# Kernel tuning notes

Measured on AMD Instinct MI355X. Metric: run time of the kernel, lower is better.

The kernel has to match this reference:

```python
import jax, jax.numpy as jnp
import numpy as np

B, S, D, H = 4, 1024, 1024, 16
DH = D // H  # 64
SCALE = 1.0 / np.sqrt(D)  # module uses 1/sqrt(d_model), not d_head


def _mh(t):
    # [B,S,D] -> [B*H,S,DH]
    b, s, _ = t.shape
    return t.reshape(b, s, H, DH).transpose(0, 2, 1, 3).reshape(b * H, s, DH)


def _shift(t):
    # pad one zero at FRONT of last dim, reinterpret (row-major) as [BH,L+1,S], drop first row
    bh, s, l = t.shape
    t = jnp.concatenate([jnp.zeros((bh, s, 1), t.dtype), t], axis=-1)
    return t.reshape(bh, l + 1, s)[:, 1:, :]


def setup_inputs() -> dict:
    key = jax.random.key(0)
    ks = jax.random.split(key, 12)
    w_sc = 1.0 / np.sqrt(D)
    return {
        "x": jax.random.normal(ks[0], (B, S, D), jnp.float32),
        "u": jax.random.normal(ks[1], (DH,), jnp.float32) * 0.02,
        "v": jax.random.normal(ks[2], (DH,), jnp.float32) * 0.02,
        "pos": jax.random.normal(ks[3], (B, S, D), jnp.float32),
        "Wq": jax.random.normal(ks[4], (D, D), jnp.float32) * w_sc,
        "bq": jnp.zeros((D,), jnp.float32),
        "Wk": jax.random.normal(ks[5], (D, D), jnp.float32) * w_sc,
        "bk": jnp.zeros((D,), jnp.float32),
        "Wv": jax.random.normal(ks[6], (D, D), jnp.float32) * w_sc,
        "bv": jnp.zeros((D,), jnp.float32),
        "Wc": jax.random.normal(ks[7], (D, D), jnp.float32) * w_sc,
        "bc": jnp.zeros((D,), jnp.float32),
    }


def reference(x, u, v, pos, Wq, bq, Wk, bk, Wv, bv, Wc, bc):
    q = _mh(x @ Wq.T + bq)      # [BH,S,DH]
    k = _mh(x @ Wk.T + bk)      # [BH,S,DH]
    w = _mh(x @ Wv.T + bv)      # [BH,S,DH]
    r = _mh(pos)                # [BH,S,DH]
    ac = jnp.einsum('bjk,bmk->bjm', q + u, k)          # content-content  [BH,S,S]
    bd = _shift(jnp.einsum('bjk,blk->bjl', q + v, r))  # content-position [BH,S,S]
    att = jax.nn.softmax((ac + bd) * SCALE, axis=-1)   # dropout is identity (eval)
    o = att @ w                                        # [BH,S,DH]
    o = o.reshape(B, H, S, DH).transpose(0, 2, 1, 3).reshape(B, S, D)
    return o @ Wc.T + bc
```

## Files before the change

kernel.cpp:

```cpp
#include <hip/hip_runtime.h>
#include <hip/hip_bf16.h>


typedef __bf16 bf16x8 __attribute__((ext_vector_type(8)));
typedef float  f32x4  __attribute__((ext_vector_type(4)));
typedef unsigned short u16x4 __attribute__((ext_vector_type(4)));

struct alignas(16) U128 { unsigned long long lo, hi; };

__device__ __forceinline__ bf16x8 ldg8(const __hip_bfloat16* p) {
    U128 u = *reinterpret_cast<const U128*>(p);
    return __builtin_bit_cast(bf16x8, u);
}

__device__ __forceinline__ __bf16 f2b(float f) {
    __hip_bfloat16 h = __float2bfloat16(f);
    return __builtin_bit_cast(__bf16, h);
}
__device__ __forceinline__ unsigned short f2bu(float f) {
    __hip_bfloat16 h = __float2bfloat16(f);
    return __builtin_bit_cast(unsigned short, h);
}
__device__ __forceinline__ float b2f(__bf16 b) {
    __hip_bfloat16 h = __builtin_bit_cast(__hip_bfloat16, b);
    return __bfloat162float(h);
}
__device__ __forceinline__ float bu2f(unsigned short u) {
    __hip_bfloat16 h = __builtin_bit_cast(__hip_bfloat16, u);
    return __bfloat162float(h);
}

__device__ __forceinline__ bf16x8 ldg8cvt(const float* p) {
    f32x4 a = *reinterpret_cast<const f32x4*>(p);
    f32x4 b = *reinterpret_cast<const f32x4*>(p + 4);
    bf16x8 r;
    r[0] = f2b(a[0]); r[1] = f2b(a[1]); r[2] = f2b(a[2]); r[3] = f2b(a[3]);
    r[4] = f2b(b[0]); r[5] = f2b(b[1]); r[6] = f2b(b[2]); r[7] = f2b(b[3]);
    return r;
}

#define MFMA16(a, b, c) __builtin_amdgcn_mfma_f32_16x16x32_bf16((a), (b), (c), 0, 0, 0)

#define C1F 0.0450843334f

__device__ __forceinline__ void gll16(const __hip_bfloat16* g, void* lds_wave_base) {
    __builtin_amdgcn_global_load_lds(
        (const __attribute__((address_space(1))) void*)g,
        (__attribute__((address_space(3))) void*)lds_wave_base,
        16, 0, 0);
}

__global__ __launch_bounds__(256) void cvt_kernel(
    const float* __restrict__ x,  const float* __restrict__ pos,
    const float* __restrict__ wq, const float* __restrict__ wk,
    const float* __restrict__ wv, const float* __restrict__ wc,
    __hip_bfloat16* __restrict__ xb, __hip_bfloat16* __restrict__ posb,
    __hip_bfloat16* __restrict__ wqkvb, __hip_bfloat16* __restrict__ wcb)
{
    const size_t base = ((size_t)blockIdx.x * 256 + threadIdx.x) * 8;
    const size_t M1 = (size_t)1 << 20;
    const float* src; __hip_bfloat16* dst; size_t o;
    if (base < 4*M1)        { src = x;   dst = xb;           o = base; }
    else if (base < 8*M1)   { src = pos; dst = posb;         o = base - 4*M1; }
    else if (base < 9*M1)   { src = wq;  dst = wqkvb;        o = base - 8*M1; }
    else if (base < 10*M1)  { src = wk;  dst = wqkvb + M1;   o = base - 9*M1; }
    else if (base < 11*M1)  { src = wv;  dst = wqkvb + 2*M1; o = base - 10*M1; }
    else                    { src = wc;  dst = wcb;          o = base - 11*M1; }
    *(bf16x8*)(dst + o) = ldg8cvt(src + o);
}

__global__ __launch_bounds__(256) void gemm_qkv(
    const __hip_bfloat16* __restrict__ A,
    const __hip_bfloat16* __restrict__ Bm,
    const float* __restrict__ bq, const float* __restrict__ bk,
    const float* __restrict__ bv, const float* __restrict__ u,
    __hip_bfloat16* __restrict__ Qu,
    __hip_bfloat16* __restrict__ Kb, __hip_bfloat16* __restrict__ Vt)
{
    __shared__ __hip_bfloat16 As[128 * 32];
    __shared__ __hip_bfloat16 Bs[128 * 32];

    const int tid  = threadIdx.x;
    const int lane = tid & 63, w = tid >> 6;
    const int quad = lane >> 4, c16 = lane & 15;
    const int wm = w >> 1, wn = w & 1;
    const int m0 = blockIdx.y * 128;
    const int n0 = blockIdx.x * 128;

    const int srow = w * 16 + (lane >> 2);
    const int scol = (lane & 3) * 8;
    const __hip_bfloat16* gA0 = A  + (size_t)(m0 + srow) * 1024 + scol;
    const __hip_bfloat16* gA1 = gA0 + (size_t)64 * 1024;
    const __hip_bfloat16* gB0 = Bm + (size_t)(n0 + srow) * 1024 + scol;
    const __hip_bfloat16* gB1 = gB0 + (size_t)64 * 1024;
    char* ldsA0 = (char*)As + (w << 10);
    char* ldsA1 = ldsA0 + 4096;
    char* ldsB0 = (char*)Bs + (w << 10);
    char* ldsB1 = ldsB0 + 4096;

    f32x4 acc[4][4] = {};

    for (int k0 = 0; k0 < 1024; k0 += 32) {
        gll16(gA0 + k0, ldsA0);
        gll16(gA1 + k0, ldsA1);
        gll16(gB0 + k0, ldsB0);
        gll16(gB1 + k0, ldsB1);
        __syncthreads();

        bf16x8 af[4], bfr[4];
        #pragma unroll
        for (int i = 0; i < 4; ++i) {
            af[i]  = *(const bf16x8*)&As[(wm * 64 + i * 16 + c16) * 32 + quad * 8];
            bfr[i] = *(const bf16x8*)&Bs[(wn * 64 + i * 16 + c16) * 32 + quad * 8];
        }
        #pragma unroll
        for (int mi = 0; mi < 4; ++mi)
            #pragma unroll
            for (int ni = 0; ni < 4; ++ni)
                acc[mi][ni] = MFMA16(af[mi], bfr[ni], acc[mi][ni]);
        __syncthreads();
    }

    #pragma unroll
    for (int mi = 0; mi < 4; ++mi) {
        #pragma unroll
        for (int ni = 0; ni < 4; ++ni) {
            const int m = m0 + wm * 64 + mi * 16 + quad * 4;
            const int n = n0 + wn * 64 + ni * 16 + c16;
            if (n < 1024) {
                const float b0 = bq[n] + u[n & 63];
                #pragma unroll
                for (int r = 0; r < 4; ++r)
                    Qu[(size_t)(m + r) * 1024 + n] =
                        __float2bfloat16((acc[mi][ni][r] + b0) * C1F);
            } else if (n < 2048) {
                const int nn = n - 1024;
                const float b0 = bk[nn];
                #pragma unroll
                for (int r = 0; r < 4; ++r)
                    Kb[(size_t)(m + r) * 1024 + nn] =
                        __float2bfloat16(acc[mi][ni][r] + b0);
            } else {
                const int nn = n - 2048;
                const float b0 = bv[nn];
                const int d = nn & 63, hh = nn >> 6;
                const int bb = m >> 10, s = m & 1023;
                u16x4 pk;
                #pragma unroll
                for (int r = 0; r < 4; ++r)
                    pk[r] = f2bu(acc[mi][ni][r] + b0);
                *(u16x4*)&Vt[(((size_t)(bb * 16 + hh) * 64 + d) << 10) + s] = pk;
            }
        }
    }
}

__global__ __launch_bounds__(256) void gemm_fin64(
    const __hip_bfloat16* __restrict__ A,
    const __hip_bfloat16* __restrict__ Bm,
    float* __restrict__ dout, const float* __restrict__ bc)
{
    __shared__ __hip_bfloat16 As[64 * 32];
    __shared__ __hip_bfloat16 Bs[64 * 32];

    const int tid  = threadIdx.x;
    const int lane = tid & 63, w = tid >> 6;
    const int quad = lane >> 4, c16 = lane & 15;
    const int wm = w >> 1, wn = w & 1;
    const int m0 = blockIdx.y * 64;
    const int n0 = blockIdx.x * 64;

    const int srow = w * 16 + (lane >> 2);
    const int scol = (lane & 3) * 8;
    const __hip_bfloat16* gA = A  + (size_t)(m0 + srow) * 1024 + scol;
    const __hip_bfloat16* gB = Bm + (size_t)(n0 + srow) * 1024 + scol;
    char* ldsA = (char*)As + (w << 10);
    char* ldsB = (char*)Bs + (w << 10);

    f32x4 acc[2][2] = {};

    for (int k0 = 0; k0 < 1024; k0 += 32) {
        gll16(gA + k0, ldsA);
        gll16(gB + k0, ldsB);
        __syncthreads();

        bf16x8 af[2], bfr[2];
        #pragma unroll
        for (int i = 0; i < 2; ++i) {
            af[i]  = *(const bf16x8*)&As[(wm * 32 + i * 16 + c16) * 32 + quad * 8];
            bfr[i] = *(const bf16x8*)&Bs[(wn * 32 + i * 16 + c16) * 32 + quad * 8];
        }
        #pragma unroll
        for (int mi = 0; mi < 2; ++mi)
            #pragma unroll
            for (int ni = 0; ni < 2; ++ni)
                acc[mi][ni] = MFMA16(af[mi], bfr[ni], acc[mi][ni]);
        __syncthreads();
    }

    #pragma unroll
    for (int mi = 0; mi < 2; ++mi) {
        #pragma unroll
        for (int ni = 0; ni < 2; ++ni) {
            const int m = m0 + wm * 32 + mi * 16 + quad * 4;
            const int n = n0 + wn * 32 + ni * 16 + c16;
            const float b0 = bc[n];
            #pragma unroll
            for (int r = 0; r < 4; ++r)
                dout[(size_t)(m + r) * 1024 + n] = acc[mi][ni][r] + b0;
        }
    }
}

__device__ __forceinline__ int lidx16(int row, int c) {
    return (row << 10) + ((((c >> 3) ^ row) << 3) | (c & 7));
}

__global__ __launch_bounds__(512, 2) void attn_kernel(
    const __hip_bfloat16* __restrict__ Qu,
    const __hip_bfloat16* __restrict__ Kb,
    const __hip_bfloat16* __restrict__ Posb,
    const __hip_bfloat16* __restrict__ Vt,
    const float* __restrict__ uvec, const float* __restrict__ vvec,
    __hip_bfloat16* __restrict__ O)
{
    __shared__ __attribute__((aligned(16))) __hip_bfloat16 Ls[64 * 1024];
    __shared__ float Wsum[64 * 8];
    __shared__ float rs[64];

    const int tid  = threadIdx.x;
    const int lane = tid & 63, w = tid >> 6;
    const int quad = lane >> 4, c16 = lane & 15;
    const int i0 = blockIdx.y * 64;
    const int bh = blockIdx.x;
    const int b = bh >> 4, h = bh & 15;
    const size_t headoff = (size_t)h * 64;
    const size_t tokbase = (size_t)b * 1024;
    const int j2 = i0 + 64;
    const bool havej2 = (j2 < 1024);

    if (tid < 64) {
        const int i = i0 + tid;
        if (i + 1 < 1024) Ls[lidx16(tid, i + 1)] = __float2bfloat16(0.f);
    }

    const __hip_bfloat16* qup0 =
        Qu + (tokbase + i0 + c16) * 1024 + headoff + quad * 8;

    float dvuA[8], dvuB[8];
    #pragma unroll
    for (int j = 0; j < 8; ++j) {
        const int d = quad * 8 + j;
        dvuA[j] = (vvec[d]      - uvec[d])      * C1F;
        dvuB[j] = (vvec[d + 32] - uvec[d + 32]) * C1F;
    }
    bf16x8 au[4][2], av[4][2];
    #pragma unroll
    for (int g = 0; g < 4; ++g) {
        au[g][0] = ldg8(qup0 + (size_t)g * 16 * 1024);
        au[g][1] = ldg8(qup0 + (size_t)g * 16 * 1024 + 32);
        #pragma unroll
        for (int j = 0; j < 8; ++j) {
            av[g][0][j] = f2b(b2f(au[g][0][j]) + dvuA[j]);
            av[g][1][j] = f2b(b2f(au[g][1][j]) + dvuB[j]);
        }
    }

    {
        bf16x8 a4[2];
        if (havej2) {
            a4[0] = ldg8(qup0 + (size_t)64 * 1024);
            a4[1] = ldg8(qup0 + (size_t)64 * 1024 + 32);
            #pragma unroll
            for (int j = 0; j < 8; ++j) {
                a4[0][j] = f2b(b2f(a4[0][j]) + dvuA[j]);
                a4[1][j] = f2b(b2f(a4[1][j]) + dvuB[j]);
            }
        }
        for (int t = 0; t < 8; ++t) {
            const int l0 = w * 128 + t * 16;
            const __hip_bfloat16* rp =
                Posb + (tokbase + l0 + c16) * 1024 + headoff + quad * 8;
            const bf16x8 r0 = ldg8(rp);
            const bf16x8 r1 = ldg8(rp + 32);
            const int lq = l0 + quad * 4;
            #pragma unroll
            for (int g = 0; g < 4; ++g) {
                f32x4 c = (f32x4){0.f, 0.f, 0.f, 0.f};
                c = MFMA16(r0, av[g][0], c);
                c = MFMA16(r1, av[g][1], c);
                const int jl = g * 16 + c16;
                const int base2 = lq + i0 + jl + 1;
                const int rwm1 = jl - 1;
                #pragma unroll
                for (int r = 0; r < 4; ++r) {
                    const int t1 = base2 + r;
                    const int cc = t1 & 1023;
                    const int rw = rwm1 + (t1 >> 10);
                    if (rw >= 0)
                        Ls[lidx16(rw, cc)] = __float2bfloat16(c[r]);
                }
            }
            if (havej2) {
                f32x4 c = (f32x4){0.f, 0.f, 0.f, 0.f};
                c = MFMA16(r0, a4[0], c);
                c = MFMA16(r1, a4[1], c);
                if (c16 == 0) {
                    #pragma unroll
                    for (int r = 0; r < 4; ++r) {
                        const int cc = lq + r + i0 + 65;
                        if (cc < 1024)
                            Ls[lidx16(63, cc)] = __float2bfloat16(c[r]);
                    }
                }
            }
        }
    }
    __syncthreads();

    {
        float rsum[4] = {0.f, 0.f, 0.f, 0.f};
        for (int t = 0; t < 8; ++t) {
            const int c0 = w * 128 + t * 16;
            const __hip_bfloat16* kp =
                Kb + (tokbase + c0 + c16) * 1024 + headoff + quad * 8;
            const bf16x8 k0 = ldg8(kp);
            const bf16x8 k1 = ldg8(kp + 32);
            const int cc0 = c0 + quad * 4;
            #pragma unroll
            for (int g = 0; g < 4; ++g) {
                f32x4 c = (f32x4){0.f, 0.f, 0.f, 0.f};
                c = MFMA16(k0, au[g][0], c);
                c = MFMA16(k1, au[g][1], c);
                const int jl = g * 16 + c16;
                const int idx = lidx16(jl, cc0);
                const u16x4 bd = *(const u16x4*)&Ls[idx];
                u16x4 pk;
                float s4 = 0.f;
                #pragma unroll
                for (int r = 0; r < 4; ++r) {
                    const float p =
                        __builtin_amdgcn_exp2f(bu2f(bd[r]) + c[r]);
                    s4 += p;
                    pk[r] = f2bu(p);
                }
                *(u16x4*)&Ls[idx] = pk;
                rsum[g] += s4;
            }
        }
        #pragma unroll
        for (int g = 0; g < 4; ++g) {
            float s = rsum[g];
            s += __shfl_xor(s, 16);
            s += __shfl_xor(s, 32);
            if (lane < 16) Wsum[(g * 16 + lane) * 8 + w] = s;
        }
    }
    __syncthreads();

    if (tid < 64) {
        float s = 0.f;
        #pragma unroll
        for (int k = 0; k < 8; ++k) s += Wsum[tid * 8 + k];
        rs[tid] = 1.f / s;
    }
    __syncthreads();

    {
        const int d0 = (w & 3) * 16;
        const int kh = w >> 2;
        const __hip_bfloat16* vp =
            Vt + ((size_t)bh * 64 + d0 + c16) * 1024 + quad * 8;
        f32x4 acc[4] = {};
        for (int kk = kh * 512; kk < kh * 512 + 512; kk += 32) {
            const bf16x8 vld = ldg8(vp + kk);
            #pragma unroll
            for (int g = 0; g < 4; ++g) {
                const bf16x8 p =
                    *(const bf16x8*)&Ls[lidx16(g * 16 + c16, kk + quad * 8)];
                acc[g] = MFMA16(p, vld, acc[g]);
            }
        }
        __syncthreads();
        float* Lf = (float*)Ls;
        const int sbase = (w & 3) * 1024;
        if (kh == 1) {
            #pragma unroll
            for (int g = 0; g < 4; ++g)
                #pragma unroll
                for (int r = 0; r < 4; ++r)
                    Lf[sbase + g * 256 + (quad * 4 + r) * 16 + c16] = acc[g][r];
        }
        __syncthreads();
        if (kh == 0) {
            #pragma unroll
            for (int g = 0; g < 4; ++g)
                #pragma unroll
                for (int r = 0; r < 4; ++r) {
                    const int il = g * 16 + quad * 4 + r;
                    const float val =
                        (acc[g][r] + Lf[sbase + g * 256 + (quad * 4 + r) * 16 + c16])
                        * rs[il];
                    const int i = i0 + il;
                    const int d = d0 + c16;
                    O[(tokbase + i) * 1024 + headoff + d] = __float2bfloat16(val);
                }
        }
    }
}

extern "C" void kernel_launch(void* const* d_in, const int* in_sizes, int n_in,
                              void* d_out, int out_size, void* d_ws, size_t ws_size,
                              hipStream_t stream)
{
    const float* x   = (const float*)d_in[0];
    const float* u   = (const float*)d_in[1];
    const float* v   = (const float*)d_in[2];
    const float* pos = (const float*)d_in[3];
    const float* Wq  = (const float*)d_in[4];
    const float* bq  = (const float*)d_in[5];
    const float* Wk  = (const float*)d_in[6];
    const float* bk  = (const float*)d_in[7];
    const float* Wv  = (const float*)d_in[8];
    const float* bv  = (const float*)d_in[9];
    const float* Wc  = (const float*)d_in[10];
    const float* bc  = (const float*)d_in[11];

    const size_t MB = (size_t)1 << 20;
    char* ws = (char*)d_ws;
    __hip_bfloat16* Qu    = (__hip_bfloat16*)(ws + 0 * MB);
    __hip_bfloat16* Kb    = (__hip_bfloat16*)(ws + 8 * MB);
    __hip_bfloat16* Vt    = (__hip_bfloat16*)(ws + 16 * MB);
    __hip_bfloat16* xb    = (__hip_bfloat16*)(ws + 24 * MB);
    __hip_bfloat16* O     = (__hip_bfloat16*)(ws + 24 * MB);
    __hip_bfloat16* Posb  = (__hip_bfloat16*)(ws + 32 * MB);
    __hip_bfloat16* Wqkvb = (__hip_bfloat16*)(ws + 40 * MB);
    __hip_bfloat16* Wcb   = (__hip_bfloat16*)(ws + 46 * MB);

    cvt_kernel<<<6144, 256, 0, stream>>>(x, pos, Wq, Wk, Wv, Wc,
                                         xb, Posb, Wqkvb, Wcb);

    gemm_qkv<<<dim3(24, 32), dim3(256), 0, stream>>>(
        xb, Wqkvb, bq, bk, bv, u, Qu, Kb, Vt);

    attn_kernel<<<dim3(64, 16), dim3(512), 0, stream>>>(
        Qu, Kb, Posb, Vt, u, v, O);

    gemm_fin64<<<dim3(16, 64), dim3(256), 0, stream>>>(
        O, Wcb, (float*)d_out, bc);
}
```

Before: 255.7 us.

## Split attention score buffer into two column halves to halve LDS footprint

The attention kernel now builds the 64x1024 shifted-position/probability tile in two 512-column phases, so the shared buffer shrinks from 128KB to 64KB. Launch bounds rise from two to four blocks per CU so more blocks can be resident. Each phase recomputes the needed position-score tiles (about 36 of 64 per phase, split unevenly across waves) and accumulates P·V across phases, with the row-sum normalisation deferred to the end. In exchange it repeats the Q/u/v loads, does some redundant position MFMAs, adds more barriers, and the higher launch bound may cause register pressure or spills.

```diff
diff --git a/kernel.cpp b/kernel.cpp
--- a/kernel.cpp
+++ b/kernel.cpp
@@ -212,11 +212,11 @@
     }
 }
 
-__device__ __forceinline__ int lidx16(int row, int c) {
-    return (row << 10) + ((((c >> 3) ^ row) << 3) | (c & 7));
-}
-
-__global__ __launch_bounds__(512, 2) void attn_kernel(
+__device__ __forceinline__ int lidx9(int row, int c) {
+    return (row << 9) + ((((c >> 3) ^ row) << 3) | (c & 7));
+}
+
+__global__ __launch_bounds__(512, 4) void attn_kernel(
     const __hip_bfloat16* __restrict__ Qu,
     const __hip_bfloat16* __restrict__ Kb,
     const __hip_bfloat16* __restrict__ Posb,
@@ -224,7 +224,7 @@
     const float* __restrict__ uvec, const float* __restrict__ vvec,
     __hip_bfloat16* __restrict__ O)
 {
-    __shared__ __attribute__((aligned(16))) __hip_bfloat16 Ls[64 * 1024];
+    __shared__ __attribute__((aligned(16))) __hip_bfloat16 Ls[64 * 512];
     __shared__ float Wsum[64 * 8];
     __shared__ float rs[64];
 
@@ -239,34 +239,46 @@
     const int j2 = i0 + 64;
     const bool havej2 = (j2 < 1024);
 
-    if (tid < 64) {
-        const int i = i0 + tid;
-        if (i + 1 < 1024) Ls[lidx16(tid, i + 1)] = __float2bfloat16(0.f);
-    }
-
     const __hip_bfloat16* qup0 =
         Qu + (tokbase + i0 + c16) * 1024 + headoff + quad * 8;
 
-    float dvuA[8], dvuB[8];
-    #pragma unroll
-    for (int j = 0; j < 8; ++j) {
-        const int d = quad * 8 + j;
-        dvuA[j] = (vvec[d]      - uvec[d])      * C1F;
-        dvuB[j] = (vvec[d + 32] - uvec[d + 32]) * C1F;
-    }
-    bf16x8 au[4][2], av[4][2];
-    #pragma unroll
-    for (int g = 0; g < 4; ++g) {
-        au[g][0] = ldg8(qup0 + (size_t)g * 16 * 1024);
-        au[g][1] = ldg8(qup0 + (size_t)g * 16 * 1024 + 32);
+    const int ntile = (w < 5) ? 5 : 4;
+    const int tbase = (w < 5) ? w * 5 : 25 + (w - 5) * 4;
+
+    f32x4 obacc[4] = {};
+    float rsum[4] = {0.f, 0.f, 0.f, 0.f};
+    const int d0 = (w & 3) * 16;
+    const int kh = w >> 2;
+    const __hip_bfloat16* vp =
+        Vt + ((size_t)bh * 64 + d0 + c16) * 1024 + quad * 8;
+
+    for (int ph = 0; ph < 2; ++ph) {
+        const int h0 = ph << 9;
+
+        if (tid < 64) {
+            const int c = i0 + tid + 1;
+            if (c < 1024 && ((c ^ h0) & 512) == 0)
+                Ls[lidx9(tid, c & 511)] = __float2bfloat16(0.f);
+        }
+
+        float dvuA[8], dvuB[8];
         #pragma unroll
         for (int j = 0; j < 8; ++j) {
-            av[g][0][j] = f2b(b2f(au[g][0][j]) + dvuA[j]);
-            av[g][1][j] = f2b(b2f(au[g][1][j]) + dvuB[j]);
-        }
-    }
-
-    {
+            const int d = quad * 8 + j;
+            dvuA[j] = (vvec[d]      - uvec[d])      * C1F;
+            dvuB[j] = (vvec[d + 32] - uvec[d + 32]) * C1F;
+        }
+        bf16x8 au[4][2], av[4][2];
+        #pragma unroll
+        for (int g = 0; g < 4; ++g) {
+            au[g][0] = ldg8(qup0 + (size_t)g * 16 * 1024);
+            au[g][1] = ldg8(qup0 + (size_t)g * 16 * 1024 + 32);
+            #pragma unroll
+            for (int j = 0; j < 8; ++j) {
+                av[g][0][j] = f2b(b2f(au[g][0][j]) + dvuA[j]);
+                av[g][1][j] = f2b(b2f(au[g][1][j]) + dvuB[j]);
+            }
+        }
         bf16x8 a4[2];
         if (havej2) {
             a4[0] = ldg8(qup0 + (size_t)64 * 1024);
@@ -277,8 +289,11 @@
                 a4[1][j] = f2b(b2f(a4[1][j]) + dvuB[j]);
             }
         }
-        for (int t = 0; t < 8; ++t) {
-            const int l0 = w * 128 + t * 16;
+
+        const int Tstart = ((h0 - i0 - 65) & 1023) >> 4;
+        for (int s = 0; s < ntile; ++s) {
+            const int tl = (Tstart + tbase + s) & 63;
+            const int l0 = tl << 4;
             const __hip_bfloat16* rp =
                 Posb + (tokbase + l0 + c16) * 1024 + headoff + quad * 8;
             const bf16x8 r0 = ldg8(rp);
@@ -297,8 +312,8 @@
                     const int t1 = base2 + r;
                     const int cc = t1 & 1023;
                     const int rw = rwm1 + (t1 >> 10);
-                    if (rw >= 0)
-                        Ls[lidx16(rw, cc)] = __float2bfloat16(c[r]);
+                    if (rw >= 0 && ((cc ^ h0) & 512) == 0)
+                        Ls[lidx9(rw, cc & 511)] = __float2bfloat16(c[r]);
                 }
             }
             if (havej2) {
@@ -308,32 +323,29 @@
                 if (c16 == 0) {
                     #pragma unroll
                     for (int r = 0; r < 4; ++r) {
-                        const int cc = lq + r + i0 + 65;
-                        if (cc < 1024)
-                            Ls[lidx16(63, cc)] = __float2bfloat16(c[r]);
+                        const int t1 = lq + r + j2 + 1;
+                        if (t1 < 1024 && ((t1 ^ h0) & 512) == 0)
+                            Ls[lidx9(63, t1 & 511)] = __float2bfloat16(c[r]);
                     }
                 }
             }
         }
-    }
-    __syncthreads();
-
-    {
-        float rsum[4] = {0.f, 0.f, 0.f, 0.f};
-        for (int t = 0; t < 8; ++t) {
-            const int c0 = w * 128 + t * 16;
+        __syncthreads();
+
+        for (int t = 0; t < 4; ++t) {
+            const int c0 = h0 + w * 64 + t * 16;
             const __hip_bfloat16* kp =
                 Kb + (tokbase + c0 + c16) * 1024 + headoff + quad * 8;
             const bf16x8 k0 = ldg8(kp);
             const bf16x8 k1 = ldg8(kp + 32);
-            const int cc0 = c0 + quad * 4;
+            const int lc0 = w * 64 + t * 16 + quad * 4;
             #pragma unroll
             for (int g = 0; g < 4; ++g) {
                 f32x4 c = (f32x4){0.f, 0.f, 0.f, 0.f};
                 c = MFMA16(k0, au[g][0], c);
                 c = MFMA16(k1, au[g][1], c);
                 const int jl = g * 16 + c16;
-                const int idx = lidx16(jl, cc0);
+                const int idx = lidx9(jl, lc0);
                 const u16x4 bd = *(const u16x4*)&Ls[idx];
                 u16x4 pk;
                 float s4 = 0.f;
@@ -348,64 +360,59 @@
                 rsum[g] += s4;
             }
         }
-        #pragma unroll
-        for (int g = 0; g < 4; ++g) {
-            float s = rsum[g];
-            s += __shfl_xor(s, 16);
-            s += __shfl_xor(s, 32);
-            if (lane < 16) Wsum[(g * 16 + lane) * 8 + w] = s;
-        }
-    }
-    __syncthreads();
-
-    if (tid < 64) {
-        float s = 0.f;
-        #pragma unroll
-        for (int k = 0; k < 8; ++k) s += Wsum[tid * 8 + k];
-        rs[tid] = 1.f / s;
-    }
-    __syncthreads();
-
-    {
-        const int d0 = (w & 3) * 16;
-        const int kh = w >> 2;
-        const __hip_bfloat16* vp =
-            Vt + ((size_t)bh * 64 + d0 + c16) * 1024 + quad * 8;
-        f32x4 acc[4] = {};
-        for (int kk = kh * 512; kk < kh * 512 + 512; kk += 32) {
-            const bf16x8 vld = ldg8(vp + kk);
+        if (ph == 1) {
+            #pragma unroll
+            for (int g = 0; g < 4; ++g) {
+                float s = rsum[g];
+                s += __shfl_xor(s, 16);
+                s += __shfl_xor(s, 32);
+                if (lane < 16) Wsum[(g * 16 + lane) * 8 + w] = s;
+            }
+        }
+        __syncthreads();
+
+        if (ph == 1 && tid < 64) {
+            float s = 0.f;
+            #pragma unroll
+            for (int k = 0; k < 8; ++k) s += Wsum[tid * 8 + k];
+            rs[tid] = 1.f / s;
+        }
+
+        for (int kk = kh * 256; kk < kh * 256 + 256; kk += 32) {
+            const bf16x8 vld = ldg8(vp + h0 + kk);
             #pragma unroll
             for (int g = 0; g < 4; ++g) {
                 const bf16x8 p =
-                    *(const bf16x8*)&Ls[lidx16(g * 16 + c16, kk + quad * 8)];
-                acc[g] = MFMA16(p, vld, acc[g]);
-            }
-        }
-        __syncthreads();
-        float* Lf = (float*)Ls;
-        const int sbase = (w & 3) * 1024;
-        if (kh == 1) {
-            #pragma unroll
-            for (int g = 0; g < 4; ++g)
-                #pragma unroll
-                for (int r = 0; r < 4; ++r)
-                    Lf[sbase + g * 256 + (quad * 4 + r) * 16 + c16] = acc[g][r];
-        }
-        __syncthreads();
-        if (kh == 0) {
-            #pragma unroll
-            for (int g = 0; g < 4; ++g)
-                #pragma unroll
-                for (int r = 0; r < 4; ++r) {
-                    const int il = g * 16 + quad * 4 + r;
-                    const float val =
-                        (acc[g][r] + Lf[sbase + g * 256 + (quad * 4 + r) * 16 + c16])
-                        * rs[il];
-                    const int i = i0 + il;
-                    const int d = d0 + c16;
-                    O[(tokbase + i) * 1024 + headoff + d] = __float2bfloat16(val);
-                }
-        }
+                    *(const bf16x8*)&Ls[lidx9(g * 16 + c16, kk + quad * 8)];
+                obacc[g] = MFMA16(p, vld, obacc[g]);
+            }
+        }
+        __syncthreads();
+    }
+
+    float* Lf = (float*)Ls;
+    const int sbase = (w & 3) * 1024;
+    if (kh == 1) {
+        #pragma unroll
+        for (int g = 0; g < 4; ++g)
+            #pragma unroll
+            for (int r = 0; r < 4; ++r)
+                Lf[sbase + g * 256 + (quad * 4 + r) * 16 + c16] = obacc[g][r];
+    }
+    __syncthreads();
+    if (kh == 0) {
+        #pragma unroll
+        for (int g = 0; g < 4; ++g)
+            #pragma unroll
+            for (int r = 0; r < 4; ++r) {
+                const int il = g * 16 + quad * 4 + r;
+                const float val =
+                    (obacc[g][r] + Lf[sbase + g * 256 + (quad * 4 + r) * 16 + c16])
+                    * rs[il];
+                const int i = i0 + il;
+                const int d = d0 + c16;
+                O[(tokbase + i) * 1024 + headoff + d] = __float2bfloat16(val);
+            }
     }
 }
 
```

Result: slower. 398.8 us (+56.0%).

## Stage V transpose through LDS and prefetch pos/K tiles in attention loops

Applied to the files above, without the earlier changes.

In the QKV GEMM epilogue, V-tile blocks now write their accumulators into a padded shared-memory tile and then emit coalesced row-contiguous stores into the transposed Vt layout. This replaces scattered 8-byte global writes, and the enlarged shared buffer raises LDS use per block. In the attention kernel, the position and key fragments for the next iteration are loaded one step ahead (software prefetch), so global load latency overlaps the MFMA work. The prefetch adds registers and one redundant wraparound load per loop.

```diff
diff --git a/kernel.cpp b/kernel.cpp
--- a/kernel.cpp
+++ b/kernel.cpp
@@ -77,8 +77,9 @@
     __hip_bfloat16* __restrict__ Qu,
     __hip_bfloat16* __restrict__ Kb, __hip_bfloat16* __restrict__ Vt)
 {
-    __shared__ __hip_bfloat16 As[128 * 32];
-    __shared__ __hip_bfloat16 Bs[128 * 32];
+    __shared__ __attribute__((aligned(16))) __hip_bfloat16 Smem[128 * 132];
+    __hip_bfloat16* As = Smem;
+    __hip_bfloat16* Bs = Smem + 4096;
 
     const int tid  = threadIdx.x;
     const int lane = tid & 63, w = tid >> 6;
@@ -121,36 +122,54 @@
         __syncthreads();
     }
 
-    #pragma unroll
-    for (int mi = 0; mi < 4; ++mi) {
+    if (n0 < 2048) {
+        #pragma unroll
+        for (int mi = 0; mi < 4; ++mi) {
+            #pragma unroll
+            for (int ni = 0; ni < 4; ++ni) {
+                const int m = m0 + wm * 64 + mi * 16 + quad * 4;
+                const int n = n0 + wn * 64 + ni * 16 + c16;
+                if (n < 1024) {
+                    const float b0 = bq[n] + u[n & 63];
+                    #pragma unroll
+                    for (int r = 0; r < 4; ++r)
+                        Qu[(size_t)(m + r) * 1024 + n] =
+                            __float2bfloat16((acc[mi][ni][r] + b0) * C1F);
+                } else {
+                    const int nn = n - 1024;
+                    const float b0 = bk[nn];
+                    #pragma unroll
+                    for (int r = 0; r < 4; ++r)
+                        Kb[(size_t)(m + r) * 1024 + nn] =
+                            __float2bfloat16(acc[mi][ni][r] + b0);
+                }
+            }
+        }
+    } else {
+        const int mlb = wm * 64 + quad * 4;
         #pragma unroll
         for (int ni = 0; ni < 4; ++ni) {
-            const int m = m0 + wm * 64 + mi * 16 + quad * 4;
-            const int n = n0 + wn * 64 + ni * 16 + c16;
-            if (n < 1024) {
-                const float b0 = bq[n] + u[n & 63];
-                #pragma unroll
-                for (int r = 0; r < 4; ++r)
-                    Qu[(size_t)(m + r) * 1024 + n] =
-                        __float2bfloat16((acc[mi][ni][r] + b0) * C1F);
-            } else if (n < 2048) {
-                const int nn = n - 1024;
-                const float b0 = bk[nn];
-                #pragma unroll
-                for (int r = 0; r < 4; ++r)
-                    Kb[(size_t)(m + r) * 1024 + nn] =
-                        __float2bfloat16(acc[mi][ni][r] + b0);
-            } else {
-                const int nn = n - 2048;
-                const float b0 = bv[nn];
-                const int d = nn & 63, hh = nn >> 6;
-                const int bb = m >> 10, s = m & 1023;
+            const int nl = wn * 64 + ni * 16 + c16;
+            const float b0 = bv[(n0 - 2048 + nl) & 1023];
+            #pragma unroll
+            for (int mi = 0; mi < 4; ++mi) {
                 u16x4 pk;
                 #pragma unroll
                 for (int r = 0; r < 4; ++r)
                     pk[r] = f2bu(acc[mi][ni][r] + b0);
-                *(u16x4*)&Vt[(((size_t)(bb * 16 + hh) * 64 + d) << 10) + s] = pk;
-            }
+                *(u16x4*)&Smem[nl * 132 + mlb + mi * 16] = pk;
+            }
+        }
+        __syncthreads();
+        const int bb = m0 >> 10;
+        const int hh0 = (n0 - 2048) >> 6;
+        const int s0 = m0 & 1023;
+        for (int i = 0; i < 32; ++i) {
+            const int nl = w * 32 + i;
+            const int R = (bb * 16 + hh0 + (nl >> 6)) * 64 + (nl & 63);
+            const unsigned int val =
+                *(const unsigned int*)&Smem[nl * 132 + lane * 2];
+            *(unsigned int*)&Vt[(size_t)R * 1024 + s0 + lane * 2] = val;
         }
     }
 }
@@ -277,13 +296,15 @@
                 a4[1][j] = f2b(b2f(a4[1][j]) + dvuB[j]);
             }
         }
+        const __hip_bfloat16* rpb =
+            Posb + (tokbase + w * 128 + c16) * 1024 + headoff + quad * 8;
+        bf16x8 r0 = ldg8(rpb);
+        bf16x8 r1 = ldg8(rpb + 32);
         for (int t = 0; t < 8; ++t) {
-            const int l0 = w * 128 + t * 16;
-            const __hip_bfloat16* rp =
-                Posb + (tokbase + l0 + c16) * 1024 + headoff + quad * 8;
-            const bf16x8 r0 = ldg8(rp);
-            const bf16x8 r1 = ldg8(rp + 32);
-            const int lq = l0 + quad * 4;
+            const int tn = (t + 1) & 7;
+            const bf16x8 p0 = ldg8(rpb + (size_t)tn * 16 * 1024);
+            const bf16x8 p1 = ldg8(rpb + (size_t)tn * 16 * 1024 + 32);
+            const int lq = w * 128 + t * 16 + quad * 4;
             #pragma unroll
             for (int g = 0; g < 4; ++g) {
                 f32x4 c = (f32x4){0.f, 0.f, 0.f, 0.f};
@@ -314,19 +335,22 @@
                     }
                 }
             }
+            r0 = p0; r1 = p1;
         }
     }
     __syncthreads();
 
     {
+        const __hip_bfloat16* kpb =
+            Kb + (tokbase + w * 128 + c16) * 1024 + headoff + quad * 8;
+        bf16x8 k0 = ldg8(kpb);
+        bf16x8 k1 = ldg8(kpb + 32);
         float rsum[4] = {0.f, 0.f, 0.f, 0.f};
         for (int t = 0; t < 8; ++t) {
-            const int c0 = w * 128 + t * 16;
-            const __hip_bfloat16* kp =
-                Kb + (tokbase + c0 + c16) * 1024 + headoff + quad * 8;
-            const bf16x8 k0 = ldg8(kp);
-            const bf16x8 k1 = ldg8(kp + 32);
-            const int cc0 = c0 + quad * 4;
+            const int tn = (t + 1) & 7;
+            const bf16x8 p0 = ldg8(kpb + (size_t)tn * 16 * 1024);
+            const bf16x8 p1 = ldg8(kpb + (size_t)tn * 16 * 1024 + 32);
+            const int cc0 = w * 128 + t * 16 + quad * 4;
             #pragma unroll
             for (int g = 0; g < 4; ++g) {
                 f32x4 c = (f32x4){0.f, 0.f, 0.f, 0.f};
@@ -347,6 +371,7 @@
                 *(u16x4*)&Ls[idx] = pk;
                 rsum[g] += s4;
             }
+            k0 = p0; k1 = p1;
         }
         #pragma unroll
         for (int g = 0; g < 4; ++g) {
```

New measurement: 249.6 us. -2.4%, faster.
